# Kernel tuning notes

Measured on AMD Instinct MI355X. Metric: run time of the kernel, lower is better.

The kernel has to match this reference:

```python
import jax, jax.numpy as jnp
import numpy as np

N_NODES = 50000
EMBED_DIM = 512
N_EDGES = 150000


def _edge_scores(node_embeddings, edges):
    # edges: [2, E] int; dot product of endpoint embeddings -> [E]
    src = node_embeddings[edges[0]]  # [E, D]
    dst = node_embeddings[edges[1]]  # [E, D]
    return jnp.sum(src * dst, axis=1)


def setup_inputs() -> dict:
    key = jax.random.key(0)
    k1, k2, k3 = jax.random.split(key, 3)
    node_embeddings = jax.random.normal(k1, (N_NODES, EMBED_DIM), dtype=jnp.float32)
    edge_index = jax.random.randint(k2, (2, N_EDGES), 0, N_NODES, dtype=jnp.int64)
    # negative edges: uniform random node pairs (matches the original sampler's
    # fallback distribution; precomputed so the reference is deterministic/jittable)
    neg_edges = jax.random.randint(k3, (2, N_EDGES), 0, N_NODES, dtype=jnp.int64)
    return {
        "node_embeddings": node_embeddings,
        "edge_index": edge_index,
        "neg_edges": neg_edges,
        "num_nodes": N_NODES,
    }


def reference(node_embeddings, edge_index, neg_edges, num_nodes):
    pos_scores = _edge_scores(node_embeddings, edge_index)  # [E]
    neg_scores = _edge_scores(node_embeddings, neg_edges)   # [E]
    all_scores = jnp.concatenate([pos_scores, neg_scores])
    all_labels = jnp.concatenate([
        jnp.ones_like(pos_scores),
        jnp.zeros_like(neg_scores),
    ])
    # BCE with logits: log(1 + exp(s)) - s*y, numerically stable via logaddexp
    per_elem = jnp.logaddexp(jnp.float32(0.0), all_scores) - all_scores * all_labels
    return jnp.mean(per_elem)
```

## Files before the change

### kernel.cpp

```cpp
#include <hip/hip_runtime.h>
#include <math.h>

#define N_EDGES   150000
#define TOTAL     300000
#define EMBED_DIM 512
#define N_NODES   50000
#define TABLE_ELEMS (N_NODES * EMBED_DIM)
#define TABLE_BYTES_F8 ((size_t)TABLE_ELEMS)
#define BLOCK_THREADS 256
#define CONV_BLOCKS 2048

#define GROUPS16   (TOTAL / 16)
#define POS_G16    (N_EDGES / 16)
#define EDGE_BLOCKS ((GROUPS16 + 3) / 4)

typedef float floatx4 __attribute__((ext_vector_type(4)));

__global__ __launch_bounds__(BLOCK_THREADS) void convert_fp8(
    const float4* __restrict__ in,
    int*          __restrict__ out,
    float*        __restrict__ acc)
{
    if (blockIdx.x == 0 && threadIdx.x == 0) *acc = 0.0f;
    const int stride = gridDim.x * blockDim.x;
    for (int i = blockIdx.x * blockDim.x + threadIdx.x;
         i < TABLE_ELEMS / 4; i += stride) {
        float4 v = in[i];
        int r = 0;
        r = __builtin_amdgcn_cvt_pk_fp8_f32(v.x, v.y, r, false);
        r = __builtin_amdgcn_cvt_pk_fp8_f32(v.z, v.w, r, true);
        out[i] = r;
    }
}

__global__ __launch_bounds__(BLOCK_THREADS, 4) void edge_loss_fp8(
    const unsigned char* __restrict__ emb8,
    const int*           __restrict__ pos_edges,
    const int*           __restrict__ neg_edges,
    float*               __restrict__ acc)
{
    const int wave = threadIdx.x >> 6;
    const int lane = threadIdx.x & 63;
    const int g    = blockIdx.x * 4 + wave;

    const int i    = lane & 15;
    const int quad = lane >> 4;
    const bool is_diag = ((i >> 2) == quad);
    const int  dreg    = i & 3;

    float contrib = 0.0f;

    if (g < GROUPS16) {
        const bool is_pos = (g < POS_G16);
        const int* __restrict__ edges = is_pos ? pos_edges : neg_edges;
        const int  e0 = 16 * g - (is_pos ? 0 : N_EDGES);

        const int sidx = edges[e0 + i];
        const int tidx = edges[N_EDGES + e0 + i];

        const unsigned long long* rA =
            (const unsigned long long*)(emb8 + (size_t)sidx * EMBED_DIM + quad * 8);
        const unsigned long long* rB =
            (const unsigned long long*)(emb8 + (size_t)tidx * EMBED_DIM + quad * 8);

        unsigned long long a[16], b[16];
        #pragma unroll
        for (int c = 0; c < 16; c++) {
            a[c] = rA[c * 4];
            b[c] = rB[c * 4];
        }

        floatx4 C0 = {0,0,0,0}, C1 = {0,0,0,0}, C2 = {0,0,0,0}, C3 = {0,0,0,0};
        #pragma unroll
        for (int c = 0; c < 4; c++) {
            C0 = __builtin_amdgcn_mfma_f32_16x16x32_fp8_fp8((long)a[c],      (long)b[c],      C0, 0, 0, 0);
            C1 = __builtin_amdgcn_mfma_f32_16x16x32_fp8_fp8((long)a[c + 4],  (long)b[c + 4],  C1, 0, 0, 0);
            C2 = __builtin_amdgcn_mfma_f32_16x16x32_fp8_fp8((long)a[c + 8],  (long)b[c + 8],  C2, 0, 0, 0);
            C3 = __builtin_amdgcn_mfma_f32_16x16x32_fp8_fp8((long)a[c + 12], (long)b[c + 12], C3, 0, 0, 0);
        }
        floatx4 C = (C0 + C1) + (C2 + C3);

        float s = (dreg == 0) ? C[0] : (dreg == 1) ? C[1] : (dreg == 2) ? C[2] : C[3];
        float sp = fmaxf(s, 0.0f) + log1pf(expf(-fabsf(s)));
        contrib = is_diag ? (sp - (is_pos ? s : 0.0f)) : 0.0f;
    }

    #pragma unroll
    for (int off = 32; off > 0; off >>= 1)
        contrib += __shfl_down(contrib, off, 64);

    __shared__ float ls[4];
    if (lane == 0) ls[wave] = contrib;
    __syncthreads();
    if (threadIdx.x == 0)
        atomicAdd(acc, ls[0] + ls[1] + ls[2] + ls[3]);
}

#define N_PAIRS   (TOTAL / 2)
#define POS_PAIRS (N_EDGES / 2)
#define FB_WAVES  (CONV_BLOCKS * 4)
__global__ __launch_bounds__(BLOCK_THREADS, 8) void edge_loss_f32(
    const float* __restrict__ emb,
    const int*   __restrict__ pos_edges,
    const int*   __restrict__ neg_edges,
    float*       __restrict__ acc)
{
    const int wave  = threadIdx.x >> 6;
    const int lane  = threadIdx.x & 63;
    const int gwave = blockIdx.x * 4 + wave;
    float lsum = 0.0f;
    for (int g = gwave; g < N_PAIRS; g += FB_WAVES) {
        const bool is_pos = (g < POS_PAIRS);
        const int* __restrict__ edges = is_pos ? pos_edges : neg_edges;
        const int  e0 = 2 * g - (is_pos ? 0 : N_EDGES);
        const int s0 = edges[e0],     t0 = edges[N_EDGES + e0];
        const int s1 = edges[e0 + 1], t1 = edges[N_EDGES + e0 + 1];
        const float4* rS0 = (const float4*)(emb + (size_t)s0 * EMBED_DIM) + lane;
        const float4* rT0 = (const float4*)(emb + (size_t)t0 * EMBED_DIM) + lane;
        const float4* rS1 = (const float4*)(emb + (size_t)s1 * EMBED_DIM) + lane;
        const float4* rT1 = (const float4*)(emb + (size_t)t1 * EMBED_DIM) + lane;
        float4 a0 = rS0[0], a1 = rS0[64];
        float4 b0 = rT0[0], b1 = rT0[64];
        float4 c0 = rS1[0], c1 = rS1[64];
        float4 d0 = rT1[0], d1 = rT1[64];
        float p0 = fmaf(a0.x, b0.x, fmaf(a0.y, b0.y, fmaf(a0.z, b0.z, a0.w * b0.w)));
        float p1 = fmaf(a1.x, b1.x, fmaf(a1.y, b1.y, fmaf(a1.z, b1.z, a1.w * b1.w)));
        float q0 = fmaf(c0.x, d0.x, fmaf(c0.y, d0.y, fmaf(c0.z, d0.z, c0.w * d0.w)));
        float q1 = fmaf(c1.x, d1.x, fmaf(c1.y, d1.y, fmaf(c1.z, d1.z, c1.w * d1.w)));
        float p = p0 + p1, q = q0 + q1;
        #pragma unroll
        for (int off = 32; off > 0; off >>= 1) {
            p += __shfl_down(p, off, 64);
            q += __shfl_down(q, off, 64);
        }
        const float sp_p = fmaxf(p, 0.0f) + log1pf(expf(-fabsf(p)));
        const float sp_q = fmaxf(q, 0.0f) + log1pf(expf(-fabsf(q)));
        lsum += (lane == 0) ? (sp_p + sp_q - (is_pos ? (p + q) : 0.0f)) : 0.0f;
    }
    __shared__ float ls[4];
    if (lane == 0) ls[wave] = lsum;
    __syncthreads();
    if (threadIdx.x == 0)
        atomicAdd(acc, ls[0] + ls[1] + ls[2] + ls[3]);
}

__global__ void finalize_kernel(const float* __restrict__ acc, float* __restrict__ out)
{
    if (threadIdx.x == 0)
        out[0] = acc[0] * (1.0f / (float)TOTAL);
}

extern "C" void kernel_launch(void* const* d_in, const int* in_sizes, int n_in,
                              void* d_out, int out_size, void* d_ws, size_t ws_size,
                              hipStream_t stream) {
    const float* emb = (const float*)d_in[0];
    const int*   pos = (const int*)d_in[1];
    const int*   neg = (const int*)d_in[2];
    float* out = (float*)d_out;

    if (ws_size >= TABLE_BYTES_F8 + 64) {
        unsigned char* emb8 = (unsigned char*)d_ws;
        float*         acc  = (float*)((char*)d_ws + TABLE_BYTES_F8);
        convert_fp8<<<CONV_BLOCKS, BLOCK_THREADS, 0, stream>>>(
            (const float4*)emb, (int*)d_ws, acc);
        edge_loss_fp8<<<EDGE_BLOCKS, BLOCK_THREADS, 0, stream>>>(emb8, pos, neg, acc);
        finalize_kernel<<<1, 64, 0, stream>>>(acc, out);
    } else {
        float* acc = (float*)d_ws;
        (void)hipMemsetAsync(acc, 0, sizeof(float), stream);
        edge_loss_f32<<<CONV_BLOCKS, BLOCK_THREADS, 0, stream>>>(emb, pos, neg, acc);
        finalize_kernel<<<1, 64, 0, stream>>>(acc, out);
    }
}
```

Baseline: 231.4 us.

## Stage gathered fp8 rows in LDS via direct global-to-LDS loads

The fp8 edge kernel now gathers the 16 source and 16 destination rows per wave into LDS using 16-byte direct global-to-LDS loads. Each row is read as one contiguous 512-byte span, replacing the earlier strided 8-byte per-lane register loads. MFMA operands are then read from LDS with an XOR-swizzled chunk index to avoid bank conflicts, and blocks shrink to two waves. The aim is better coalescing and fewer memory transactions on the random row gather, at the cost of 32 KB LDS per block, which limits occupancy.

```diff
diff --git a/kernel.cpp b/kernel.cpp
--- a/kernel.cpp
+++ b/kernel.cpp
@@ -7,16 +7,18 @@
 #define N_NODES   50000
 #define TABLE_ELEMS (N_NODES * EMBED_DIM)
 #define TABLE_BYTES_F8 ((size_t)TABLE_ELEMS)
-#define BLOCK_THREADS 256
 #define CONV_BLOCKS 2048
+#define CONV_THREADS 256
 
 #define GROUPS16   (TOTAL / 16)
 #define POS_G16    (N_EDGES / 16)
-#define EDGE_BLOCKS ((GROUPS16 + 3) / 4)
+#define EDGE_THREADS 128
+#define EDGE_BLOCKS (GROUPS16 / 2)
 
 typedef float floatx4 __attribute__((ext_vector_type(4)));
+union I4 { int4 v; long long l[2]; };
 
-__global__ __launch_bounds__(BLOCK_THREADS) void convert_fp8(
+__global__ __launch_bounds__(CONV_THREADS) void convert_fp8(
     const float4* __restrict__ in,
     int*          __restrict__ out,
     float*        __restrict__ acc)
@@ -33,73 +35,88 @@
     }
 }
 
-__global__ __launch_bounds__(BLOCK_THREADS, 4) void edge_loss_fp8(
+__global__ __launch_bounds__(EDGE_THREADS) void edge_loss_fp8_lds(
     const unsigned char* __restrict__ emb8,
     const int*           __restrict__ pos_edges,
     const int*           __restrict__ neg_edges,
     float*               __restrict__ acc)
 {
+    __shared__ __align__(16) char smem[2][16384];
+
     const int wave = threadIdx.x >> 6;
     const int lane = threadIdx.x & 63;
-    const int g    = blockIdx.x * 4 + wave;
+    const int g    = blockIdx.x * 2 + wave;
 
-    const int i    = lane & 15;
+    const int r    = lane & 15;
     const int quad = lane >> 4;
-    const bool is_diag = ((i >> 2) == quad);
-    const int  dreg    = i & 3;
 
-    float contrib = 0.0f;
+    const bool is_pos = (g < POS_G16);
+    const int* __restrict__ edges = is_pos ? pos_edges : neg_edges;
+    const int  e0 = 16 * g - (is_pos ? 0 : N_EDGES);
 
-    if (g < GROUPS16) {
-        const bool is_pos = (g < POS_G16);
-        const int* __restrict__ edges = is_pos ? pos_edges : neg_edges;
-        const int  e0 = 16 * g - (is_pos ? 0 : N_EDGES);
+    const int sidx = edges[e0 + r];
+    const int tidx = edges[N_EDGES + e0 + r];
 
-        const int sidx = edges[e0 + i];
-        const int tidx = edges[N_EDGES + e0 + i];
+    char* wbase = smem[wave];
+    const int  lo5 = lane & 31;
+    const bool hi  = lane >= 32;
 
-        const unsigned long long* rA =
-            (const unsigned long long*)(emb8 + (size_t)sidx * EMBED_DIM + quad * 8);
-        const unsigned long long* rB =
-            (const unsigned long long*)(emb8 + (size_t)tidx * EMBED_DIM + quad * 8);
+    #pragma unroll
+    for (int p = 0; p < 16; p++) {
+        const int srow = __builtin_amdgcn_readlane(sidx, p);
+        const int trow = __builtin_amdgcn_readlane(tidx, p);
+        const int row  = hi ? trow : srow;
+        const unsigned char* gp = emb8 + (size_t)row * EMBED_DIM + lo5 * 16;
+#if __has_builtin(__builtin_amdgcn_global_load_lds)
+        __builtin_amdgcn_global_load_lds(
+            (const __attribute__((address_space(1))) unsigned int*)gp,
+            (__attribute__((address_space(3))) unsigned int*)(wbase + p * 1024),
+            16, 0, 0);
+#else
+        *(int4*)(wbase + p * 1024 + lane * 16) = *(const int4*)gp;
+#endif
+    }
+#if __has_builtin(__builtin_amdgcn_global_load_lds)
+    __builtin_amdgcn_s_waitcnt(0x0f70);
+#endif
 
-        unsigned long long a[16], b[16];
-        #pragma unroll
-        for (int c = 0; c < 16; c++) {
-            a[c] = rA[c * 4];
-            b[c] = rB[c * 4];
+    floatx4 Ca = {0,0,0,0}, Cb = {0,0,0,0}, Cc = {0,0,0,0}, Cd = {0,0,0,0};
+    #pragma unroll
+    for (int c = 0; c < 8; c++) {
+        const int m = ((c << 2) + quad) ^ r;
+        const char* lp = wbase + r * 1024 + m * 16;
+        I4 a, b;
+        a.v = *(const int4*)lp;
+        b.v = *(const int4*)(lp + 512);
+        if (c & 1) {
+            Cc = __builtin_amdgcn_mfma_f32_16x16x32_fp8_fp8(a.l[0], b.l[0], Cc, 0, 0, 0);
+            Cd = __builtin_amdgcn_mfma_f32_16x16x32_fp8_fp8(a.l[1], b.l[1], Cd, 0, 0, 0);
+        } else {
+            Ca = __builtin_amdgcn_mfma_f32_16x16x32_fp8_fp8(a.l[0], b.l[0], Ca, 0, 0, 0);
+            Cb = __builtin_amdgcn_mfma_f32_16x16x32_fp8_fp8(a.l[1], b.l[1], Cb, 0, 0, 0);
         }
+    }
+    const floatx4 C = (Ca + Cb) + (Cc + Cd);
 
-        floatx4 C0 = {0,0,0,0}, C1 = {0,0,0,0}, C2 = {0,0,0,0}, C3 = {0,0,0,0};
-        #pragma unroll
-        for (int c = 0; c < 4; c++) {
-            C0 = __builtin_amdgcn_mfma_f32_16x16x32_fp8_fp8((long)a[c],      (long)b[c],      C0, 0, 0, 0);
-            C1 = __builtin_amdgcn_mfma_f32_16x16x32_fp8_fp8((long)a[c + 4],  (long)b[c + 4],  C1, 0, 0, 0);
-            C2 = __builtin_amdgcn_mfma_f32_16x16x32_fp8_fp8((long)a[c + 8],  (long)b[c + 8],  C2, 0, 0, 0);
-            C3 = __builtin_amdgcn_mfma_f32_16x16x32_fp8_fp8((long)a[c + 12], (long)b[c + 12], C3, 0, 0, 0);
-        }
-        floatx4 C = (C0 + C1) + (C2 + C3);
-
-        float s = (dreg == 0) ? C[0] : (dreg == 1) ? C[1] : (dreg == 2) ? C[2] : C[3];
-        float sp = fmaxf(s, 0.0f) + log1pf(expf(-fabsf(s)));
-        contrib = is_diag ? (sp - (is_pos ? s : 0.0f)) : 0.0f;
-    }
+    const int dreg = r & 3;
+    const float s  = (dreg == 0) ? C[0] : (dreg == 1) ? C[1] : (dreg == 2) ? C[2] : C[3];
+    const float sp = fmaxf(s, 0.0f) + log1pf(expf(-fabsf(s)));
+    float contrib  = ((r >> 2) == quad) ? (sp - (is_pos ? s : 0.0f)) : 0.0f;
 
     #pragma unroll
     for (int off = 32; off > 0; off >>= 1)
         contrib += __shfl_down(contrib, off, 64);
 
-    __shared__ float ls[4];
-    if (lane == 0) ls[wave] = contrib;
+    if (lane == 0) *(float*)wbase = contrib;
     __syncthreads();
     if (threadIdx.x == 0)
-        atomicAdd(acc, ls[0] + ls[1] + ls[2] + ls[3]);
+        atomicAdd(acc, *(const float*)smem[0] + *(const float*)smem[1]);
 }
 
 #define N_PAIRS   (TOTAL / 2)
 #define POS_PAIRS (N_EDGES / 2)
 #define FB_WAVES  (CONV_BLOCKS * 4)
-__global__ __launch_bounds__(BLOCK_THREADS, 8) void edge_loss_f32(
+__global__ __launch_bounds__(CONV_THREADS, 8) void edge_loss_f32(
     const float* __restrict__ emb,
     const int*   __restrict__ pos_edges,
     const int*   __restrict__ neg_edges,
@@ -115,10 +132,10 @@
         const int  e0 = 2 * g - (is_pos ? 0 : N_EDGES);
         const int s0 = edges[e0],     t0 = edges[N_EDGES + e0];
         const int s1 = edges[e0 + 1], t1 = edges[N_EDGES + e0 + 1];
-        const float4* rS0 = (const float4*)(emb + (size_t)s0 * EMBED_DIM) + lane;
-        const float4* rT0 = (const float4*)(emb + (size_t)t0 * EMBED_DIM) + lane;
-        const float4* rS1 = (const float4*)(emb + (size_t)s1 * EMBED_DIM) + lane;
-        const float4* rT1 = (const float4*)(emb + (size_t)t1 * EMBED_DIM) + lane;
+        const float4* rS0 = (const float4*)(emb + (size_t)s0 * 512) + lane;
+        const float4* rT0 = (const float4*)(emb + (size_t)t0 * 512) + lane;
+        const float4* rS1 = (const float4*)(emb + (size_t)s1 * 512) + lane;
+        const float4* rT1 = (const float4*)(emb + (size_t)t1 * 512) + lane;
         float4 a0 = rS0[0], a1 = rS0[64];
         float4 b0 = rT0[0], b1 = rT0[64];
         float4 c0 = rS1[0], c1 = rS1[64];
@@ -161,14 +178,14 @@
     if (ws_size >= TABLE_BYTES_F8 + 64) {
         unsigned char* emb8 = (unsigned char*)d_ws;
         float*         acc  = (float*)((char*)d_ws + TABLE_BYTES_F8);
-        convert_fp8<<<CONV_BLOCKS, BLOCK_THREADS, 0, stream>>>(
+        convert_fp8<<<CONV_BLOCKS, CONV_THREADS, 0, stream>>>(
             (const float4*)emb, (int*)d_ws, acc);
-        edge_loss_fp8<<<EDGE_BLOCKS, BLOCK_THREADS, 0, stream>>>(emb8, pos, neg, acc);
+        edge_loss_fp8_lds<<<EDGE_BLOCKS, EDGE_THREADS, 0, stream>>>(emb8, pos, neg, acc);
         finalize_kernel<<<1, 64, 0, stream>>>(acc, out);
     } else {
         float* acc = (float*)d_ws;
         (void)hipMemsetAsync(acc, 0, sizeof(float), stream);
-        edge_loss_f32<<<CONV_BLOCKS, BLOCK_THREADS, 0, stream>>>(emb, pos, neg, acc);
+        edge_loss_f32<<<CONV_BLOCKS, CONV_THREADS, 0, stream>>>(emb, pos, neg, acc);
         finalize_kernel<<<1, 64, 0, stream>>>(acc, out);
     }
 }
```

Result: slower. 280.9 us (+21.4%).
